# Performance work log

Hardware: AMD Instinct MI355X
Metric: run time of the kernel (lower is better)

The kernel has to match this reference:

```python
import jax, jax.numpy as jnp
import numpy as np

B, S, D, H = 4, 2048, 1024, 16
HD = D // H  # head_dim = 64
SCALE = 1.0 / np.sqrt(HD)
NEG = -1e9


def setup_inputs() -> dict:
    key = jax.random.key(0)
    ks = jax.random.split(key, 8)
    return {
        "query": jax.random.normal(ks[0], (B, S, D), jnp.float32),
        "key": jax.random.normal(ks[1], (B, S, D), jnp.float32),
        "value": jax.random.normal(ks[2], (B, S, D), jnp.float32),
        "mask": jax.random.randint(ks[3], (B, 1, S, S), 0, 2, jnp.int32),
        "Wq": jax.random.normal(ks[4], (D, D), jnp.float32) * 0.02,
        "Wk": jax.random.normal(ks[5], (D, D), jnp.float32) * 0.02,
        "Wv": jax.random.normal(ks[6], (D, D), jnp.float32) * 0.02,
        "Wo": jax.random.normal(ks[7], (D, D), jnp.float32) * 0.02,
    }


def _split_heads(x):
    # [B,S,D] -> [B,H,S,HD]
    b, s, _ = x.shape
    return x.reshape(b, s, H, HD).transpose(0, 2, 1, 3)


def reference(query, key, value, mask, Wq, Wk, Wv, Wo):
    # nn.Linear(d,d,bias=False): y = x @ W.T ; here Wq etc. are the weight matrices.
    q = _split_heads(query @ Wq.T)
    k = _split_heads(key @ Wk.T)
    v = _split_heads(value @ Wv.T)
    scores = jnp.einsum("bhqd,bhkd->bhqk", q, k) * SCALE
    scores = jnp.where(mask == 0, NEG, scores)
    probs = jax.nn.softmax(scores, axis=-1)  # dropout p=0 (eval) -> identity
    attn = jnp.einsum("bhqk,bhkd->bhqd", probs, v)
    attn = attn.transpose(0, 2, 1, 3).reshape(query.shape[0], query.shape[1], D)
    return attn @ Wo.T
```

## Files before the change

kernel.cpp:

```cpp
#include <hip/hip_runtime.h>
#include <hip/hip_bf16.h>
#include <stdint.h>


typedef unsigned short u16;
typedef __bf16  bf16x8 __attribute__((ext_vector_type(8)));
typedef float   fx4    __attribute__((ext_vector_type(4)));
typedef u16     u16x4v __attribute__((ext_vector_type(4)));
typedef u16     u16x8v __attribute__((ext_vector_type(8)));

#define MFMA16(a, b, c) __builtin_amdgcn_mfma_f32_16x16x32_bf16(a, b, c, 0, 0, 0)

__device__ __forceinline__ u16 f2bf(float f) {
    __bf16 b = (__bf16)f;
    return __builtin_bit_cast(unsigned short, b);
}

__device__ __forceinline__ void gload_lds16(const void* g, void* l) {
    auto gp = (const __attribute__((address_space(1))) unsigned int*)(uintptr_t)g;
    auto lp = (__attribute__((address_space(3))) unsigned int*)(unsigned int)(uintptr_t)l;
    __builtin_amdgcn_global_load_lds(gp, lp, 16, 0, 0);
}

__global__ __launch_bounds__(256) void cast3_k(const float* __restrict__ s0,
                                               const float* __restrict__ s1,
                                               const float* __restrict__ s2,
                                               u16* __restrict__ d0,
                                               u16* __restrict__ d1,
                                               u16* __restrict__ d2, int n8) {
    int i = blockIdx.x * 256 + threadIdx.x;
    if (i >= n8) return;
    const float* s = (blockIdx.y == 0) ? s0 : (blockIdx.y == 1) ? s1 : s2;
    u16* d = (blockIdx.y == 0) ? d0 : (blockIdx.y == 1) ? d1 : d2;
    const float4* s4 = (const float4*)s;
    float4 a = s4[(size_t)i * 2];
    float4 b = s4[(size_t)i * 2 + 1];
    u16x8v o;
    o[0] = f2bf(a.x); o[1] = f2bf(a.y); o[2] = f2bf(a.z); o[3] = f2bf(a.w);
    o[4] = f2bf(b.x); o[5] = f2bf(b.y); o[6] = f2bf(b.z); o[7] = f2bf(b.w);
    *(u16x8v*)(d + (size_t)i * 8) = o;
}

__global__ __launch_bounds__(256) void castw_k(const float* __restrict__ s0,
                                               const float* __restrict__ s1,
                                               const float* __restrict__ s2,
                                               const float* __restrict__ s3,
                                               u16* __restrict__ d0,
                                               u16* __restrict__ d1,
                                               u16* __restrict__ d2,
                                               u16* __restrict__ d3, int n8) {
    int i = blockIdx.x * 256 + threadIdx.x;
    if (i >= n8) return;
    const float* s = (blockIdx.y == 0) ? s0 : (blockIdx.y == 1) ? s1
                   : (blockIdx.y == 2) ? s2 : s3;
    u16* d = (blockIdx.y == 0) ? d0 : (blockIdx.y == 1) ? d1
           : (blockIdx.y == 2) ? d2 : d3;
    float sc = (blockIdx.y == 0) ? 0.1803368801111204f : 1.0f;
    const float4* s4 = (const float4*)s;
    float4 a = s4[(size_t)i * 2];
    float4 b = s4[(size_t)i * 2 + 1];
    u16x8v o;
    o[0] = f2bf(a.x * sc); o[1] = f2bf(a.y * sc); o[2] = f2bf(a.z * sc); o[3] = f2bf(a.w * sc);
    o[4] = f2bf(b.x * sc); o[5] = f2bf(b.y * sc); o[6] = f2bf(b.z * sc); o[7] = f2bf(b.w * sc);
    *(u16x8v*)(d + (size_t)i * 8) = o;
}

__global__ __launch_bounds__(256) void pack_mask_k(const int* __restrict__ m,
                                                   unsigned long long* __restrict__ o,
                                                   int nw) {
    int t = blockIdx.x * 256 + threadIdx.x;
    int wid = t >> 6;
    if (wid >= nw) return;
    int v = m[(size_t)wid * 64 + (t & 63)];
    unsigned long long bits = __ballot(v != 0);
    if ((t & 63) == 0) o[wid] = bits;
}

template <int MODE>
__global__ __launch_bounds__(256) void gemm_bt(const u16* __restrict__ A,
                                               const u16* __restrict__ Bw,
                                               void* __restrict__ Cp,
                                               int M, int N, int K) {
    __shared__ __align__(16) u16 As[128 * 32];
    __shared__ __align__(16) u16 Bs[128 * 32];
    const int tid = threadIdx.x;
    const int w = tid >> 6, l = tid & 63, lg = l >> 4, lr = l & 15;
    const int wr = w >> 1, wc = w & 1;
    const int nb = N >> 7;
    const int nwg = gridDim.x;
    const int sw = (blockIdx.x & 7) * (nwg >> 3) + (blockIdx.x >> 3);
    const int bm = sw / nb, bn = sw % nb;

    fx4 acc[4][4] = {};

    const int id0 = tid, id1 = 256 + tid;
    const int r0 = id0 >> 2, k80 = (id0 & 3) * 8;
    const int r1 = id1 >> 2, k81 = (id1 & 3) * 8;
    const u16* Ab = A + (size_t)(bm * 128) * K;
    const u16* Bb = Bw + (size_t)(bn * 128) * K;
    char* AsW0 = (char*)As + (w * 64) * 16;
    char* AsW1 = (char*)As + (256 + w * 64) * 16;
    char* BsW0 = (char*)Bs + (w * 64) * 16;
    char* BsW1 = (char*)Bs + (256 + w * 64) * 16;

    for (int k0 = 0; k0 < K; k0 += 32) {
        __syncthreads();
        gload_lds16(Ab + (size_t)r0 * K + k0 + k80, AsW0);
        gload_lds16(Ab + (size_t)r1 * K + k0 + k81, AsW1);
        gload_lds16(Bb + (size_t)r0 * K + k0 + k80, BsW0);
        gload_lds16(Bb + (size_t)r1 * K + k0 + k81, BsW1);
        __syncthreads();
        bf16x8 af[4], bf[4];
#pragma unroll
        for (int m = 0; m < 4; ++m)
            af[m] = *(const bf16x8*)(As + (wr * 64 + m * 16 + lr) * 32 + lg * 8);
#pragma unroll
        for (int n = 0; n < 4; ++n)
            bf[n] = *(const bf16x8*)(Bs + (wc * 64 + n * 16 + lr) * 32 + lg * 8);
#pragma unroll
        for (int m = 0; m < 4; ++m)
#pragma unroll
            for (int n = 0; n < 4; ++n)
                acc[m][n] = MFMA16(af[m], bf[n], acc[m][n]);
    }

    if (MODE == 2) {
        float* Cf = (float*)Cp;
#pragma unroll
        for (int m = 0; m < 4; ++m) {
#pragma unroll
            for (int n = 0; n < 4; ++n) {
                int c = bn * 128 + wc * 64 + n * 16 + lr;
#pragma unroll
                for (int j = 0; j < 4; ++j) {
                    int r = bm * 128 + wr * 64 + m * 16 + lg * 4 + j;
                    Cf[(size_t)r * N + c] = acc[m][n][j];
                }
            }
        }
    } else if (MODE == 0) {
        u16* Cb = (u16*)Cp;
#pragma unroll
        for (int m = 0; m < 4; ++m) {
#pragma unroll
            for (int n = 0; n < 4; ++n) {
                int c = bn * 128 + wc * 64 + n * 16 + lr;
                int hh = c >> 6, hd = c & 63;
#pragma unroll
                for (int j = 0; j < 4; ++j) {
                    int r = bm * 128 + wr * 64 + m * 16 + lg * 4 + j;
                    int bb = r >> 11, s = r & 2047;
                    Cb[((size_t)(bb * 16 + hh) * 2048 + s) * 64 + hd] =
                        f2bf(acc[m][n][j]);
                }
            }
        }
    } else {
        u16* Cb = (u16*)Cp;
#pragma unroll
        for (int m = 0; m < 4; ++m) {
            int rb = bm * 128 + wr * 64 + m * 16 + lg * 4;
            int bb = rb >> 11, s0 = rb & 2047;
#pragma unroll
            for (int n = 0; n < 4; ++n) {
                int c = bn * 128 + wc * 64 + n * 16 + lr;
                int hh = c >> 6, hd = c & 63;
                u16x4v pk;
#pragma unroll
                for (int j = 0; j < 4; ++j) pk[j] = f2bf(acc[m][n][j]);
                *(u16x4v*)(Cb + ((size_t)(bb * 16 + hh) * 64 + hd) * 2048 + s0) = pk;
            }
        }
    }
}

__global__ __launch_bounds__(256) void attn_k(const u16* __restrict__ qh,
                                              const u16* __restrict__ kh,
                                              const u16* __restrict__ vt,
                                              const unsigned long long* __restrict__ mb,
                                              u16* __restrict__ out) {
    __shared__ __align__(16) u16 Ks[64 * 64];
    __shared__ __align__(16) u16 Vs[64 * 64];
    __shared__ __align__(16) u16 Ps[4][32 * 64];

    const int tid = threadIdx.x;
    const int w = tid >> 6, l = tid & 63, lg = l >> 4, lr = l & 15;
    const int lg4 = lg * 4;
    const int sw0 = (blockIdx.x & 7) * 128 + (blockIdx.x >> 3);
    const int qt = sw0 & 15;
    const int bh = sw0 >> 4;
    const int bb = bh >> 4, hh = bh & 15;

    const u16* qp = qh + (size_t)bh * 2048 * 64;
    const u16* kp = kh + (size_t)bh * 2048 * 64;
    const u16* vp = vt + (size_t)bh * 64 * 2048;
    const unsigned long long* mbp = mb + (size_t)bb * 2048 * 32;

    const int qrow0 = qt * 128 + w * 32;

    bf16x8 qf[2][2];
#pragma unroll
    for (int st = 0; st < 2; ++st) {
        const u16* qr = qp + (size_t)(qrow0 + st * 16 + lr) * 64;
        qf[st][0] = *(const bf16x8*)(qr + lg * 8);
        qf[st][1] = *(const bf16x8*)(qr + 32 + lg * 8);
    }

    fx4 accO[2][4] = {};
    fx4 lsum[2] = {};
    float mrun[2] = {-INFINITY, -INFINITY};

    u16x8v ov;
#pragma unroll
    for (int i = 0; i < 8; ++i) ov[i] = 0x3F80;
    const bf16x8 ones = __builtin_bit_cast(bf16x8, ov);

    u16* pw = Ps[w];
    const int swl = (lr & 7) << 4;

    const int sr0 = tid >> 3,         sc0 = (tid & 7) * 8;
    const int sr1 = (256 + tid) >> 3, sc1 = (tid & 7) * 8;
    const int lb0 = sr0 * 128 + ((sc0 * 2) ^ ((sr0 & 7) << 4));
    const int lb1 = sr1 * 128 + ((sc1 * 2) ^ ((sr1 & 7) << 4));

    bf16x8 kr0 = *(const bf16x8*)(kp + (size_t)sr0 * 64 + sc0);
    bf16x8 kr1 = *(const bf16x8*)(kp + (size_t)sr1 * 64 + sc1);
    bf16x8 vr0 = *(const bf16x8*)(vp + (size_t)sr0 * 2048 + sc0);
    bf16x8 vr1 = *(const bf16x8*)(vp + (size_t)sr1 * 2048 + sc1);

    for (int kt = 0; kt < 32; ++kt) {
        uint2 mw0 = *(const uint2*)(mbp + (size_t)(qrow0 + lr) * 32 + kt);
        uint2 mw1 = *(const uint2*)(mbp + (size_t)(qrow0 + 16 + lr) * 32 + kt);

        __syncthreads();
        *(bf16x8*)((char*)Ks + lb0) = kr0;
        *(bf16x8*)((char*)Ks + lb1) = kr1;
        *(bf16x8*)((char*)Vs + lb0) = vr0;
        *(bf16x8*)((char*)Vs + lb1) = vr1;
        __syncthreads();

        if (kt < 31) {
            const u16* kpn = kp + (size_t)(kt + 1) * 64 * 64;
            kr0 = *(const bf16x8*)(kpn + (size_t)sr0 * 64 + sc0);
            kr1 = *(const bf16x8*)(kpn + (size_t)sr1 * 64 + sc1);
            vr0 = *(const bf16x8*)(vp + (size_t)sr0 * 2048 + (kt + 1) * 64 + sc0);
            vr1 = *(const bf16x8*)(vp + (size_t)sr1 * 2048 + (kt + 1) * 64 + sc1);
        }

        fx4 sa[2][4];
#pragma unroll
        for (int nf = 0; nf < 4; ++nf) {
            int kk = nf * 16 + lr;
            int rb = kk * 128, sw = (kk & 7) << 4;
            bf16x8 kf0 = *(const bf16x8*)((const char*)Ks + rb + ((lg * 16) ^ sw));
            bf16x8 kf1 = *(const bf16x8*)((const char*)Ks + rb + ((64 + lg * 16) ^ sw));
#pragma unroll
            for (int st = 0; st < 2; ++st) {
                fx4 a = {0.f, 0.f, 0.f, 0.f};
                a = MFMA16(kf0, qf[st][0], a);
                a = MFMA16(kf1, qf[st][1], a);
                sa[st][nf] = a;
            }
        }

        float mt[2];
#pragma unroll
        for (int st = 0; st < 2; ++st) {
            float m01 = fmaxf(fmaxf(sa[st][0][0], sa[st][0][1]), fmaxf(sa[st][0][2], sa[st][0][3]));
            float m23 = fmaxf(fmaxf(sa[st][1][0], sa[st][1][1]), fmaxf(sa[st][1][2], sa[st][1][3]));
            float m45 = fmaxf(fmaxf(sa[st][2][0], sa[st][2][1]), fmaxf(sa[st][2][2], sa[st][2][3]));
            float m67 = fmaxf(fmaxf(sa[st][3][0], sa[st][3][1]), fmaxf(sa[st][3][2], sa[st][3][3]));
            float m = fmaxf(fmaxf(m01, m23), fmaxf(m45, m67));
            m = fmaxf(m, __shfl_xor(m, 16));
            m = fmaxf(m, __shfl_xor(m, 32));
            mt[st] = m;
        }

        if (!__all(mt[0] <= mrun[0] + 8.f && mt[1] <= mrun[1] + 8.f)) {
#pragma unroll
            for (int st = 0; st < 2; ++st) {
                float mnew = fmaxf(mrun[st], mt[st]);
                float f = exp2f(mrun[st] - mnew);
                mrun[st] = mnew;
#pragma unroll
                for (int j = 0; j < 4; ++j) {
                    float fj = __shfl(f, lg4 + j);
                    lsum[st][j] *= fj;
#pragma unroll
                    for (int ff = 0; ff < 4; ++ff) accO[st][ff][j] *= fj;
                }
            }
        }

#pragma unroll
        for (int st = 0; st < 2; ++st) {
            uint2 mw = st ? mw1 : mw0;
            int rowb = (st * 16 + lr) * 128;
#pragma unroll
            for (int nf = 0; nf < 4; ++nf) {
                unsigned wv = (nf & 2) ? mw.y : mw.x;
                int pos0 = (nf & 1) * 16 + lg4;
                u16x4v pk;
#pragma unroll
                for (int r = 0; r < 4; ++r) {
                    float p = exp2f(sa[st][nf][r] - mrun[st]);
                    int keep = __builtin_amdgcn_sbfe((int)wv, pos0 + r, 1);
                    p = __builtin_bit_cast(float,
                            __builtin_bit_cast(int, p) & keep);
                    pk[r] = f2bf(p);
                }
                *(u16x4v*)((char*)pw + rowb + ((nf * 32 + lg4 * 2) ^ swl)) = pk;
            }
        }

#pragma unroll
        for (int ks = 0; ks < 2; ++ks) {
            int pco = (ks * 64 + lg * 16);
            bf16x8 pa0 = *(const bf16x8*)((const char*)pw + lr * 128 + (pco ^ swl));
            bf16x8 pa1 = *(const bf16x8*)((const char*)pw + (16 + lr) * 128 + (pco ^ swl));
            lsum[0] = MFMA16(pa0, ones, lsum[0]);
            lsum[1] = MFMA16(pa1, ones, lsum[1]);
#pragma unroll
            for (int f = 0; f < 4; ++f) {
                int d = f * 16 + lr;
                int vb = d * 128 + (pco ^ ((d & 7) << 4));
                bf16x8 vv = *(const bf16x8*)((const char*)Vs + vb);
                accO[0][f] = MFMA16(pa0, vv, accO[0][f]);
                accO[1][f] = MFMA16(pa1, vv, accO[1][f]);
            }
        }
    }

#pragma unroll
    for (int st = 0; st < 2; ++st) {
#pragma unroll
        for (int j = 0; j < 4; ++j) {
            float rinv = 1.0f / lsum[st][j];
            int s = qrow0 + st * 16 + lg4 + j;
#pragma unroll
            for (int f = 0; f < 4; ++f) {
                float o = accO[st][f][j] * rinv;
                out[(size_t)(bb * 2048 + s) * 1024 + hh * 64 + f * 16 + lr] = f2bf(o);
            }
        }
    }
}

extern "C" void kernel_launch(void* const* d_in, const int* in_sizes, int n_in,
                              void* d_out, int out_size, void* d_ws, size_t ws_size,
                              hipStream_t stream) {
    const float* Qin = (const float*)d_in[0];
    const float* Kin = (const float*)d_in[1];
    const float* Vin = (const float*)d_in[2];
    const int*   Mk  = (const int*)d_in[3];
    const float* Wq  = (const float*)d_in[4];
    const float* Wk  = (const float*)d_in[5];
    const float* Wv  = (const float*)d_in[6];
    const float* Wo  = (const float*)d_in[7];

    const size_t NX = (size_t)4 * 2048 * 1024;
    const size_t NW = (size_t)1024 * 1024;

    char* ws = (char*)d_ws;
    size_t off = 0;
    auto carve = [&](size_t bytes) -> char* {
        char* p = ws + off;
        off += (bytes + 255) & ~(size_t)255;
        return p;
    };
    u16* xq = (u16*)carve(NX * 2);
    u16* xk = (u16*)carve(NX * 2);
    u16* xv = (u16*)carve(NX * 2);
    u16* wq = (u16*)carve(NW * 2);
    u16* wk = (u16*)carve(NW * 2);
    u16* wv = (u16*)carve(NW * 2);
    u16* wo = (u16*)carve(NW * 2);
    u16* qh = (u16*)carve(NX * 2);
    u16* kh = (u16*)carve(NX * 2);
    u16* vtb = (u16*)carve(NX * 2);
    unsigned long long* mbits = (unsigned long long*)carve((size_t)4 * 2048 * 32 * 8);
    u16* am = (u16*)carve(NX * 2);

    cast3_k<<<dim3(4096, 3), 256, 0, stream>>>(Qin, Kin, Vin, xq, xk, xv,
                                               (int)(NX / 8));
    castw_k<<<dim3(512, 4), 256, 0, stream>>>(Wq, Wk, Wv, Wo, wq, wk, wv, wo,
                                              (int)(NW / 8));
    pack_mask_k<<<65536, 256, 0, stream>>>(Mk, mbits, 4 * 2048 * 32);

    gemm_bt<0><<<512, 256, 0, stream>>>(xq, wq, qh, 8192, 1024, 1024);
    gemm_bt<0><<<512, 256, 0, stream>>>(xk, wk, kh, 8192, 1024, 1024);
    gemm_bt<1><<<512, 256, 0, stream>>>(xv, wv, vtb, 8192, 1024, 1024);

    attn_k<<<1024, 256, 0, stream>>>(qh, kh, vtb, mbits, am);

    gemm_bt<2><<<512, 256, 0, stream>>>(am, wo, d_out, 8192, 1024, 1024);
}
```

Measured before the change: 484.4 us.

## Double-buffer GEMM and attention LDS tiles; keep P in registers via permlane

The GEMM and attention kernels now use two LDS buffers filled by direct global-to-LDS loads, so the next K/V or A/B tile streams in while the current one is computed, with one barrier per iteration. The attention kernel drops the per-tile max reduction and rescale. It uses a fixed running offset and only rescales by 2^-64 when the row sums get close to overflow. P is repacked into MFMA operand layout with v_permlane32_swap and shuffles instead of a round trip through LDS. This saves LDS traffic and barriers but leans on the score range staying bounded, and it doubles LDS use per block.

```diff
diff --git a/kernel.cpp b/kernel.cpp
--- a/kernel.cpp
+++ b/kernel.cpp
@@ -8,12 +8,19 @@
 typedef float   fx4    __attribute__((ext_vector_type(4)));
 typedef u16     u16x4v __attribute__((ext_vector_type(4)));
 typedef u16     u16x8v __attribute__((ext_vector_type(8)));
+typedef unsigned int uint4v __attribute__((ext_vector_type(4)));
 
 #define MFMA16(a, b, c) __builtin_amdgcn_mfma_f32_16x16x32_bf16(a, b, c, 0, 0, 0)
 
 __device__ __forceinline__ u16 f2bf(float f) {
     __bf16 b = (__bf16)f;
     return __builtin_bit_cast(unsigned short, b);
+}
+__device__ __forceinline__ unsigned pk2(float lo, float hi) {
+    return (unsigned)f2bf(lo) | ((unsigned)f2bf(hi) << 16);
+}
+__device__ __forceinline__ void plane32_swap(unsigned& a, unsigned& b) {
+    asm volatile("v_permlane32_swap_b32 %0, %1" : "+v"(a), "+v"(b));
 }
 
 __device__ __forceinline__ void gload_lds16(const void* g, void* l) {
@@ -81,8 +88,8 @@
                                                const u16* __restrict__ Bw,
                                                void* __restrict__ Cp,
                                                int M, int N, int K) {
-    __shared__ __align__(16) u16 As[128 * 32];
-    __shared__ __align__(16) u16 Bs[128 * 32];
+    __shared__ __align__(16) u16 As[2][128 * 32];
+    __shared__ __align__(16) u16 Bs[2][128 * 32];
     const int tid = threadIdx.x;
     const int w = tid >> 6, l = tid & 63, lg = l >> 4, lr = l & 15;
     const int wr = w >> 1, wc = w & 1;
@@ -93,35 +100,39 @@
 
     fx4 acc[4][4] = {};
 
-    const int id0 = tid, id1 = 256 + tid;
-    const int r0 = id0 >> 2, k80 = (id0 & 3) * 8;
-    const int r1 = id1 >> 2, k81 = (id1 & 3) * 8;
+    const int r0 = tid >> 2, k8 = (tid & 3) * 8;
+    const int r1 = 64 + r0;
     const u16* Ab = A + (size_t)(bm * 128) * K;
     const u16* Bb = Bw + (size_t)(bn * 128) * K;
-    char* AsW0 = (char*)As + (w * 64) * 16;
-    char* AsW1 = (char*)As + (256 + w * 64) * 16;
-    char* BsW0 = (char*)Bs + (w * 64) * 16;
-    char* BsW1 = (char*)Bs + (256 + w * 64) * 16;
-
+
+    auto STAGE = [&](int k0, int b) {
+        char* A0 = (char*)As[b] + w * 1024;
+        char* B0 = (char*)Bs[b] + w * 1024;
+        gload_lds16(Ab + (size_t)r0 * K + k0 + k8, A0);
+        gload_lds16(Ab + (size_t)r1 * K + k0 + k8, A0 + 4096);
+        gload_lds16(Bb + (size_t)r0 * K + k0 + k8, B0);
+        gload_lds16(Bb + (size_t)r1 * K + k0 + k8, B0 + 4096);
+    };
+
+    STAGE(0, 0);
+    __syncthreads();
+    int cur = 0;
     for (int k0 = 0; k0 < K; k0 += 32) {
-        __syncthreads();
-        gload_lds16(Ab + (size_t)r0 * K + k0 + k80, AsW0);
-        gload_lds16(Ab + (size_t)r1 * K + k0 + k81, AsW1);
-        gload_lds16(Bb + (size_t)r0 * K + k0 + k80, BsW0);
-        gload_lds16(Bb + (size_t)r1 * K + k0 + k81, BsW1);
-        __syncthreads();
+        if (k0 + 32 < K) STAGE(k0 + 32, cur ^ 1);
         bf16x8 af[4], bf[4];
 #pragma unroll
         for (int m = 0; m < 4; ++m)
-            af[m] = *(const bf16x8*)(As + (wr * 64 + m * 16 + lr) * 32 + lg * 8);
+            af[m] = *(const bf16x8*)(As[cur] + (wr * 64 + m * 16 + lr) * 32 + lg * 8);
 #pragma unroll
         for (int n = 0; n < 4; ++n)
-            bf[n] = *(const bf16x8*)(Bs + (wc * 64 + n * 16 + lr) * 32 + lg * 8);
+            bf[n] = *(const bf16x8*)(Bs[cur] + (wc * 64 + n * 16 + lr) * 32 + lg * 8);
 #pragma unroll
         for (int m = 0; m < 4; ++m)
 #pragma unroll
             for (int n = 0; n < 4; ++n)
                 acc[m][n] = MFMA16(af[m], bf[n], acc[m][n]);
+        __syncthreads();
+        cur ^= 1;
     }
 
     if (MODE == 2) {
@@ -174,14 +185,13 @@
     }
 }
 
-__global__ __launch_bounds__(256) void attn_k(const u16* __restrict__ qh,
-                                              const u16* __restrict__ kh,
-                                              const u16* __restrict__ vt,
-                                              const unsigned long long* __restrict__ mb,
-                                              u16* __restrict__ out) {
-    __shared__ __align__(16) u16 Ks[64 * 64];
-    __shared__ __align__(16) u16 Vs[64 * 64];
-    __shared__ __align__(16) u16 Ps[4][32 * 64];
+__global__ __launch_bounds__(256, 4) void attn_k(const u16* __restrict__ qh,
+                                                 const u16* __restrict__ kh,
+                                                 const u16* __restrict__ vt,
+                                                 const unsigned long long* __restrict__ mb,
+                                                 u16* __restrict__ out) {
+    __shared__ __align__(16) u16 Ks[2][64 * 64];
+    __shared__ __align__(16) u16 Vs[2][64 * 64];
 
     const int tid = threadIdx.x;
     const int w = tid >> 6, l = tid & 63, lg = l >> 4, lr = l & 15;
@@ -208,127 +218,118 @@
 
     fx4 accO[2][4] = {};
     fx4 lsum[2] = {};
-    float mrun[2] = {-INFINITY, -INFINITY};
+    float mrun[2] = {0.f, 0.f};
 
     u16x8v ov;
 #pragma unroll
     for (int i = 0; i < 8; ++i) ov[i] = 0x3F80;
     const bf16x8 ones = __builtin_bit_cast(bf16x8, ov);
 
-    u16* pw = Ps[w];
-    const int swl = (lr & 7) << 4;
-
-    const int sr0 = tid >> 3,         sc0 = (tid & 7) * 8;
-    const int sr1 = (256 + tid) >> 3, sc1 = (tid & 7) * 8;
-    const int lb0 = sr0 * 128 + ((sc0 * 2) ^ ((sr0 & 7) << 4));
-    const int lb1 = sr1 * 128 + ((sc1 * 2) ^ ((sr1 & 7) << 4));
-
-    bf16x8 kr0 = *(const bf16x8*)(kp + (size_t)sr0 * 64 + sc0);
-    bf16x8 kr1 = *(const bf16x8*)(kp + (size_t)sr1 * 64 + sc1);
-    bf16x8 vr0 = *(const bf16x8*)(vp + (size_t)sr0 * 2048 + sc0);
-    bf16x8 vr1 = *(const bf16x8*)(vp + (size_t)sr1 * 2048 + sc1);
+    const int r0 = tid >> 3, r1 = 32 + r0;
+    const int sb = ((tid & 7) * 16) ^ ((r0 & 7) << 4);
+    auto STAGE = [&](int kt, int b) {
+        char* kd = (char*)Ks[b] + w * 1024;
+        char* vd = (char*)Vs[b] + w * 1024;
+        gload_lds16((const char*)kp + ((size_t)(kt * 64 + r0) * 128 + sb), kd);
+        gload_lds16((const char*)kp + ((size_t)(kt * 64 + r1) * 128 + sb), kd + 4096);
+        gload_lds16((const char*)vp + ((size_t)r0 * 4096 + (size_t)kt * 128 + sb), vd);
+        gload_lds16((const char*)vp + ((size_t)r1 * 4096 + (size_t)kt * 128 + sb), vd + 4096);
+    };
+
+    STAGE(0, 0);
+    __syncthreads();
+    int cur = 0;
 
     for (int kt = 0; kt < 32; ++kt) {
         uint2 mw0 = *(const uint2*)(mbp + (size_t)(qrow0 + lr) * 32 + kt);
         uint2 mw1 = *(const uint2*)(mbp + (size_t)(qrow0 + 16 + lr) * 32 + kt);
-
-        __syncthreads();
-        *(bf16x8*)((char*)Ks + lb0) = kr0;
-        *(bf16x8*)((char*)Ks + lb1) = kr1;
-        *(bf16x8*)((char*)Vs + lb0) = vr0;
-        *(bf16x8*)((char*)Vs + lb1) = vr1;
-        __syncthreads();
-
-        if (kt < 31) {
-            const u16* kpn = kp + (size_t)(kt + 1) * 64 * 64;
-            kr0 = *(const bf16x8*)(kpn + (size_t)sr0 * 64 + sc0);
-            kr1 = *(const bf16x8*)(kpn + (size_t)sr1 * 64 + sc1);
-            vr0 = *(const bf16x8*)(vp + (size_t)sr0 * 2048 + (kt + 1) * 64 + sc0);
-            vr1 = *(const bf16x8*)(vp + (size_t)sr1 * 2048 + (kt + 1) * 64 + sc1);
-        }
-
-        fx4 sa[2][4];
+        if (kt < 31) STAGE(kt + 1, cur ^ 1);
+
+        unsigned pw0[2][4], pw1[2][4];
+        const char* Kc = (const char*)Ks[cur];
 #pragma unroll
         for (int nf = 0; nf < 4; ++nf) {
             int kk = nf * 16 + lr;
-            int rb = kk * 128, sw = (kk & 7) << 4;
-            bf16x8 kf0 = *(const bf16x8*)((const char*)Ks + rb + ((lg * 16) ^ sw));
-            bf16x8 kf1 = *(const bf16x8*)((const char*)Ks + rb + ((64 + lg * 16) ^ sw));
+            int rb = kk * 128, swz = (kk & 7) << 4;
+            bf16x8 kf0 = *(const bf16x8*)(Kc + rb + ((lg * 16) ^ swz));
+            bf16x8 kf1 = *(const bf16x8*)(Kc + rb + ((64 + lg * 16) ^ swz));
 #pragma unroll
             for (int st = 0; st < 2; ++st) {
                 fx4 a = {0.f, 0.f, 0.f, 0.f};
                 a = MFMA16(kf0, qf[st][0], a);
                 a = MFMA16(kf1, qf[st][1], a);
-                sa[st][nf] = a;
-            }
-        }
-
-        float mt[2];
-#pragma unroll
-        for (int st = 0; st < 2; ++st) {
-            float m01 = fmaxf(fmaxf(sa[st][0][0], sa[st][0][1]), fmaxf(sa[st][0][2], sa[st][0][3]));
-            float m23 = fmaxf(fmaxf(sa[st][1][0], sa[st][1][1]), fmaxf(sa[st][1][2], sa[st][1][3]));
-            float m45 = fmaxf(fmaxf(sa[st][2][0], sa[st][2][1]), fmaxf(sa[st][2][2], sa[st][2][3]));
-            float m67 = fmaxf(fmaxf(sa[st][3][0], sa[st][3][1]), fmaxf(sa[st][3][2], sa[st][3][3]));
-            float m = fmaxf(fmaxf(m01, m23), fmaxf(m45, m67));
-            m = fmaxf(m, __shfl_xor(m, 16));
-            m = fmaxf(m, __shfl_xor(m, 32));
-            mt[st] = m;
-        }
-
-        if (!__all(mt[0] <= mrun[0] + 8.f && mt[1] <= mrun[1] + 8.f)) {
-#pragma unroll
-            for (int st = 0; st < 2; ++st) {
-                float mnew = fmaxf(mrun[st], mt[st]);
-                float f = exp2f(mrun[st] - mnew);
-                mrun[st] = mnew;
-#pragma unroll
-                for (int j = 0; j < 4; ++j) {
-                    float fj = __shfl(f, lg4 + j);
-                    lsum[st][j] *= fj;
-#pragma unroll
-                    for (int ff = 0; ff < 4; ++ff) accO[st][ff][j] *= fj;
-                }
-            }
-        }
-
-#pragma unroll
-        for (int st = 0; st < 2; ++st) {
-            uint2 mw = st ? mw1 : mw0;
-            int rowb = (st * 16 + lr) * 128;
-#pragma unroll
-            for (int nf = 0; nf < 4; ++nf) {
+                uint2 mw = st ? mw1 : mw0;
                 unsigned wv = (nf & 2) ? mw.y : mw.x;
                 int pos0 = (nf & 1) * 16 + lg4;
-                u16x4v pk;
+                float p[4];
 #pragma unroll
                 for (int r = 0; r < 4; ++r) {
-                    float p = exp2f(sa[st][nf][r] - mrun[st]);
+                    float e = exp2f(a[r] - mrun[st]);
                     int keep = __builtin_amdgcn_sbfe((int)wv, pos0 + r, 1);
-                    p = __builtin_bit_cast(float,
-                            __builtin_bit_cast(int, p) & keep);
-                    pk[r] = f2bf(p);
+                    p[r] = __builtin_bit_cast(float,
+                               __builtin_bit_cast(int, e) & keep);
                 }
-                *(u16x4v*)((char*)pw + rowb + ((nf * 32 + lg4 * 2) ^ swl)) = pk;
-            }
-        }
-
+                pw0[st][nf] = pk2(p[0], p[1]);
+                pw1[st][nf] = pk2(p[2], p[3]);
+            }
+        }
+
+        bf16x8 pa[2][2];
+        const bool odd = (lg & 1) != 0;
+#pragma unroll
+        for (int st = 0; st < 2; ++st) {
+#pragma unroll
+            for (int ks = 0; ks < 2; ++ks) {
+                unsigned x0 = pw0[st][2 * ks], y0 = pw0[st][2 * ks + 1];
+                unsigned x1 = pw1[st][2 * ks], y1 = pw1[st][2 * ks + 1];
+                plane32_swap(x0, y0);
+                plane32_swap(x1, y1);
+                unsigned x0s = (unsigned)__shfl_xor((int)x0, 16);
+                unsigned y0s = (unsigned)__shfl_xor((int)y0, 16);
+                unsigned x1s = (unsigned)__shfl_xor((int)x1, 16);
+                unsigned y1s = (unsigned)__shfl_xor((int)y1, 16);
+                uint4v wds;
+                wds[0] = odd ? y0s : x0;
+                wds[1] = odd ? y1s : x1;
+                wds[2] = odd ? y0 : x0s;
+                wds[3] = odd ? y1 : x1s;
+                pa[st][ks] = __builtin_bit_cast(bf16x8, wds);
+            }
+        }
+
+        const char* Vc = (const char*)Vs[cur];
 #pragma unroll
         for (int ks = 0; ks < 2; ++ks) {
-            int pco = (ks * 64 + lg * 16);
-            bf16x8 pa0 = *(const bf16x8*)((const char*)pw + lr * 128 + (pco ^ swl));
-            bf16x8 pa1 = *(const bf16x8*)((const char*)pw + (16 + lr) * 128 + (pco ^ swl));
-            lsum[0] = MFMA16(pa0, ones, lsum[0]);
-            lsum[1] = MFMA16(pa1, ones, lsum[1]);
+            lsum[0] = MFMA16(pa[0][ks], ones, lsum[0]);
+            lsum[1] = MFMA16(pa[1][ks], ones, lsum[1]);
 #pragma unroll
             for (int f = 0; f < 4; ++f) {
                 int d = f * 16 + lr;
-                int vb = d * 128 + (pco ^ ((d & 7) << 4));
-                bf16x8 vv = *(const bf16x8*)((const char*)Vs + vb);
-                accO[0][f] = MFMA16(pa0, vv, accO[0][f]);
-                accO[1][f] = MFMA16(pa1, vv, accO[1][f]);
-            }
-        }
+                int vb = d * 128 + ((ks * 64 + lg * 16) ^ ((d & 7) << 4));
+                bf16x8 vv = *(const bf16x8*)(Vc + vb);
+                accO[0][f] = MFMA16(pa[0][ks], vv, accO[0][f]);
+                accO[1][f] = MFMA16(pa[1][ks], vv, accO[1][f]);
+            }
+        }
+
+        float lmx = fmaxf(fmaxf(fmaxf(lsum[0][0], lsum[0][1]), fmaxf(lsum[0][2], lsum[0][3])),
+                          fmaxf(fmaxf(lsum[1][0], lsum[1][1]), fmaxf(lsum[1][2], lsum[1][3])));
+        if (!__all(lmx < 1.8446744e19f)) {
+            const float dn = 5.421010862427522e-20f;
+            mrun[0] += 64.f; mrun[1] += 64.f;
+#pragma unroll
+            for (int st = 0; st < 2; ++st) {
+#pragma unroll
+                for (int j = 0; j < 4; ++j) {
+                    lsum[st][j] *= dn;
+#pragma unroll
+                    for (int f = 0; f < 4; ++f) accO[st][f][j] *= dn;
+                }
+            }
+        }
+
+        __syncthreads();
+        cur ^= 1;
     }
 
 #pragma unroll
```

Result: faster. 444.8 us (-8.2%).
